# Performance work log

Measured on AMD Instinct MI355X. Metric: run time of the kernel, lower is better.

Reference implementation:

```python
import jax, jax.numpy as jnp
import numpy as np

B, S, H = 1, 2048, 2048
NH, NKV, HD = 32, 4, 128
G = NH // NKV            # query groups per kv head
EPS = 1e-6
THETA = 1000000.0


def _rmsnorm(x, w):
    # per-head RMSNorm over last (head_dim) axis
    var = jnp.mean(jnp.square(x), axis=-1, keepdims=True)
    return x * jax.lax.rsqrt(var + EPS) * w


def _rotate_half(x):
    x1, x2 = jnp.split(x, 2, axis=-1)
    return jnp.concatenate([-x2, x1], axis=-1)


def _rope(x, cos, sin):
    # x: [B,S,h,HD], cos/sin: [S,HD]
    c = cos[None, :, None, :]
    s = sin[None, :, None, :]
    return x * c + _rotate_half(x) * s


def setup_inputs() -> dict:
    key = jax.random.key(0)
    ks = jax.random.split(key, 7)
    inv_freq = 1.0 / (THETA ** (jnp.arange(0, HD, 2, dtype=jnp.float32) / HD))
    freqs = jnp.outer(jnp.arange(S, dtype=jnp.float32), inv_freq)  # [S, HD/2]
    emb = jnp.concatenate([freqs, freqs], axis=-1)                 # [S, HD]
    std = 0.02
    return {
        "hidden_states": jax.random.normal(ks[0], (B, S, H), jnp.float32),
        "wq": jax.random.normal(ks[1], (H, NH * HD), jnp.float32) * std,
        "wk": jax.random.normal(ks[2], (H, NKV * HD), jnp.float32) * std,
        "wv": jax.random.normal(ks[3], (H, NKV * HD), jnp.float32) * std,
        "wo": jax.random.normal(ks[4], (NH * HD, H), jnp.float32) * std,
        "q_norm_w": jnp.ones((HD,), jnp.float32),
        "k_norm_w": jnp.ones((HD,), jnp.float32),
        "cos": jnp.cos(emb),
        "sin": jnp.sin(emb),
    }


def reference(hidden_states, wq, wk, wv, wo, q_norm_w, k_norm_w, cos, sin):
    b, s, _ = hidden_states.shape
    q = (hidden_states @ wq).reshape(b, s, NH, HD)
    k = (hidden_states @ wk).reshape(b, s, NKV, HD)
    v = (hidden_states @ wv).reshape(b, s, NKV, HD)
    # QK per-head RMSNorm, then interleaved RoPE (rotate-half form)
    q = _rope(_rmsnorm(q, q_norm_w), cos, sin)
    k = _rope(_rmsnorm(k, k_norm_w), cos, sin)
    # GQA: group Q heads per KV head instead of materializing repeated K/V
    qg = q.reshape(b, s, NKV, G, HD)
    scaling = HD ** -0.5
    scores = jnp.einsum('bqhgd,bkhd->bhgqk', qg, k) * scaling  # [B,NKV,G,S,S]
    causal = jnp.tril(jnp.ones((s, s), bool))
    scores = jnp.where(causal, scores, jnp.finfo(scores.dtype).min)
    p = jax.nn.softmax(scores, axis=-1)
    attn = jnp.einsum('bhgqk,bkhd->bqhgd', p, v).reshape(b, s, NH * HD)
    return attn @ wo
```

## Files before the change

### kernel.cpp

```cpp
#include <hip/hip_runtime.h>
#include <hip/hip_bf16.h>
#include <stdint.h>

#define SEQ 2048
#define HDIM 128
#define NHEADS 32
#define NKVH 4

typedef unsigned short u16;
typedef __bf16 bf16_t;
typedef bf16_t bf16x8 __attribute__((ext_vector_type(8)));
typedef float floatx4 __attribute__((ext_vector_type(4)));

__device__ __forceinline__ float bf2f(u16 u) {
  union { uint32_t i; float f; } v; v.i = ((uint32_t)u) << 16; return v.f;
}
__device__ __forceinline__ u16 f2bf(float f) {
  if (__builtin_isnan(f)) return 0;
  union { float f; uint32_t i; } v; v.f = f;
  uint32_t r = v.i + 0x7fffu + ((v.i >> 16) & 1u);
  return (u16)(r >> 16);
}
__device__ __forceinline__ float loadf_any(const void* p, size_t i, int isbf) {
  return isbf ? bf2f(((const u16*)p)[i]) : ((const float*)p)[i];
}

__device__ __forceinline__ void gload_lds16(const u16* g, u16* l) {
  __builtin_amdgcn_global_load_lds((__attribute__((address_space(1))) void*)g,
                                   (__attribute__((address_space(3))) void*)l,
                                   16, 0, 0);
}

__device__ __forceinline__ floatx4 mfma16(bf16x8 a, bf16x8 b, floatx4 c) {
  return __builtin_amdgcn_mfma_f32_16x16x32_bf16(a, b, c, 0, 0, 0);
}

struct InPack { const u16* p[9]; int n[9]; };

__global__ void detect_all(InPack pk, int* __restrict__ flags) {
  const int which = blockIdx.x;
  const u16* x = pk.p[which];
  const int n = pk.n[which];
  __shared__ int s_sane, s_zeven, s_zodd;
  if (threadIdx.x == 0) { s_sane = 0; s_zeven = 0; s_zodd = 0; }
  __syncthreads();
  const int ns = n < 8192 ? n : 8192;
  int sane = 0, zeven = 0, zodd = 0;
  for (int i = threadIdx.x; i < ns; i += 256) {
    const u16 u = x[i];
    const int e = (u >> 7) & 0xff;
    if ((e >= 96 && e <= 159) || u == 0) sane++;
    if (u == 0) { if (i & 1) zodd++; else zeven++; }
  }
#pragma unroll
  for (int off = 32; off >= 1; off >>= 1) {
    sane += __shfl_xor(sane, off, 64);
    zeven += __shfl_xor(zeven, off, 64);
    zodd += __shfl_xor(zodd, off, 64);
  }
  if ((threadIdx.x & 63) == 0) {
    atomicAdd(&s_sane, sane);
    atomicAdd(&s_zeven, zeven);
    atomicAdd(&s_zodd, zodd);
  }
  __syncthreads();
  if (threadIdx.x == 0) {
    const int even = (ns + 1) / 2, odd = ns / 2;
    const bool mostly_sane = (s_sane * 10 >= ns * 9);
    const bool fp32_const_pattern = (s_zeven * 2 >= even) && (s_zodd * 10 <= odd);
    flags[which] = (mostly_sane && !fp32_const_pattern) ? 1 : 0;
    if (which == 0) flags[15] = 1;
  }
}

__global__ __launch_bounds__(256) void convert_any(
    const void* __restrict__ in, u16* __restrict__ out, int n,
    const int* __restrict__ flag) {
  const int isbf = *flag;
  const int i = blockIdx.x * 256 + threadIdx.x;
  if (i >= n) return;
  out[i] = isbf ? ((const u16*)in)[i] : f2bf(((const float*)in)[i]);
}

__global__ __launch_bounds__(256) void transpose_any(
    const void* __restrict__ in, u16* __restrict__ out, int R, int C,
    const int* __restrict__ flag) {
  __shared__ u16 tile[64][65];
  const int isbf = *flag;
  const int c0 = blockIdx.x * 64, r0 = blockIdx.y * 64;
  const int t = threadIdx.x;
#pragma unroll
  for (int i = 0; i < 16; i++) {
    const int idx = i * 256 + t;
    const int r = idx >> 6, c = idx & 63;
    tile[r][c] = (u16)(isbf ? ((const u16*)in)[(size_t)(r0 + r) * C + c0 + c]
                            : f2bf(((const float*)in)[(size_t)(r0 + r) * C + c0 + c]));
  }
  __syncthreads();
#pragma unroll
  for (int i = 0; i < 16; i++) {
    const int idx = i * 256 + t;
    const int cc = idx >> 6, rr = idx & 63;
    out[(size_t)(c0 + cc) * R + r0 + rr] = tile[rr][cc];
  }
}

__global__ __launch_bounds__(256) void gemm_bt_bf16(
    const u16* __restrict__ A, const u16* __restrict__ BT,
    void* __restrict__ C, int M, int N, int K,
    const int* __restrict__ cflag) {
  __shared__ alignas(16) u16 As[128 * 32];
  __shared__ alignas(16) u16 Bs[128 * 32];
  const int t = threadIdx.x;
  const int w = t >> 6;
  const int lane = t & 63;
  const int lhi = lane >> 4, llo = lane & 15;
  const int m0 = blockIdx.y * 128, n0 = blockIdx.x * 128;
  const int wm = (w & 1) * 64, wn = (w >> 1) * 64;

  floatx4 acc[4][4];
#pragma unroll
  for (int i = 0; i < 4; i++)
#pragma unroll
    for (int j = 0; j < 4; j++) acc[i][j] = (floatx4)(0.0f);

  for (int k0 = 0; k0 < K; k0 += 32) {
#pragma unroll
    for (int r = 0; r < 2; r++) {
      const int c = r * 256 + t;
      const int row = c >> 2, kc = c & 3;
      const int base = (r * 256 + w * 64) * 8;
      gload_lds16(A + (size_t)(m0 + row) * K + k0 + kc * 8, &As[base]);
      gload_lds16(BT + (size_t)(n0 + row) * K + k0 + kc * 8, &Bs[base]);
    }
    __syncthreads();
    bf16x8 af[4], bfr[4];
#pragma unroll
    for (int i = 0; i < 4; i++)
      af[i] = *(const bf16x8*)&As[(wm + i * 16 + llo) * 32 + lhi * 8];
#pragma unroll
    for (int j = 0; j < 4; j++)
      bfr[j] = *(const bf16x8*)&Bs[(wn + j * 16 + llo) * 32 + lhi * 8];
#pragma unroll
    for (int i = 0; i < 4; i++)
#pragma unroll
      for (int j = 0; j < 4; j++)
        acc[i][j] = mfma16(af[i], bfr[j], acc[i][j]);
    __syncthreads();
  }
  const int cbf = *cflag;
#pragma unroll
  for (int i = 0; i < 4; i++) {
    const int row0 = m0 + wm + i * 16 + lhi * 4;
#pragma unroll
    for (int j = 0; j < 4; j++) {
      const int col = n0 + wn + j * 16 + llo;
#pragma unroll
      for (int r = 0; r < 4; r++) {
        if (cbf) ((u16*)C)[(size_t)(row0 + r) * N + col] = f2bf(acc[i][j][r]);
        else ((float*)C)[(size_t)(row0 + r) * N + col] = acc[i][j][r];
      }
    }
  }
}

__global__ __launch_bounds__(128) void norm_rope_inplace(
    u16* __restrict__ QKV,
    const void* __restrict__ qw, const void* __restrict__ kw,
    const void* __restrict__ cosb, const void* __restrict__ sinb,
    const int* __restrict__ flags) {
  const int qwbf = flags[5], kwbf = flags[6], cbf = flags[7], sbf = flags[8];
  const int s = blockIdx.x, hy = blockIdx.y, d = threadIdx.x;
  const bool isQ = hy < NHEADS;
  const int col = isQ ? hy * HDIM : 4096 + (hy - NHEADS) * HDIM;
  u16* ptr = QKV + (size_t)s * 5120 + col + d;
  const float x = bf2f(*ptr);
  float v = x * x;
#pragma unroll
  for (int off = 32; off >= 1; off >>= 1) v += __shfl_xor(v, off, 64);
  __shared__ float sw[2];
  __shared__ float sh[128];
  if ((d & 63) == 0) sw[d >> 6] = v;
  __syncthreads();
  const float mean = (sw[0] + sw[1]) * (1.0f / 128.0f);
  const float rn = rsqrtf(mean + 1e-6f);
  const float wv = isQ ? loadf_any(qw, d, qwbf) : loadf_any(kw, d, kwbf);
  const float xn = x * rn * wv;
  sh[d] = xn;
  __syncthreads();
  const float other = sh[d ^ 64];
  const float cv = loadf_any(cosb, (size_t)s * HDIM + d, cbf);
  const float sv = loadf_any(sinb, (size_t)s * HDIM + d, sbf);
  const float o = xn * cv + (d < 64 ? -other : other) * sv;
  *ptr = f2bf(o);
}

__global__ __launch_bounds__(256) void v_transpose(
    const u16* __restrict__ QKV, u16* __restrict__ Vt) {
  __shared__ u16 tile[64][65];
  const int s0 = blockIdx.x * 64, d0 = blockIdx.y * 64, hk = blockIdx.z;
  const int t = threadIdx.x;
#pragma unroll
  for (int i = 0; i < 16; i++) {
    const int idx = i * 256 + t;
    const int r = idx >> 6, c = idx & 63;
    tile[r][c] = QKV[(size_t)(s0 + r) * 5120 + 4608 + hk * HDIM + d0 + c];
  }
  __syncthreads();
#pragma unroll
  for (int i = 0; i < 16; i++) {
    const int idx = i * 256 + t;
    const int dd = idx >> 6, ss = idx & 63;
    Vt[((size_t)hk * HDIM + d0 + dd) * SEQ + s0 + ss] = tile[ss][dd];
  }
}

__global__ __launch_bounds__(256) void flash_attn(
    const u16* __restrict__ QKV, const u16* __restrict__ Vt,
    u16* __restrict__ O) {
  __shared__ alignas(16) u16 Klds[64 * 128];
  __shared__ alignas(16) u16 Vlds[128 * 64];
  __shared__ alignas(16) u16 Plds[4][32 * 72];
  const int t = threadIdx.x;
  const int w = t >> 6;
  const int lane = t & 63;
  const int lhi = lane >> 4, llo = lane & 15;
  const int b = blockIdx.x;
  const int qt = (SEQ / 128 - 1) - (b >> 5);
  const int h = b & 31, hk = h >> 3;
  const int q0 = qt * 128;
  const int qw0 = q0 + w * 32;
  const float scale = 0.08838834764831845f;
  const float SMAX = 16.0f;

  bf16x8 qf[2][4];
#pragma unroll
  for (int i = 0; i < 2; i++)
#pragma unroll
    for (int c = 0; c < 4; c++)
      qf[i][c] = *(const bf16x8*)(QKV + (size_t)(qw0 + i * 16 + llo) * 5120 +
                                  h * HDIM + c * 32 + lhi * 8);

  floatx4 oacc[2][8];
  float lacc[2][4];
#pragma unroll
  for (int i = 0; i < 2; i++) {
#pragma unroll
    for (int d = 0; d < 8; d++) oacc[i][d] = (floatx4)(0.0f);
#pragma unroll
    for (int r = 0; r < 4; r++) lacc[i][r] = 0.0f;
  }

  const int ntiles = 2 * qt + 2;
  for (int tt = 0; tt < ntiles; tt++) {
    const int kv0 = tt * 64;
#pragma unroll
    for (int r = 0; r < 4; r++) {
      const int c = r * 256 + t;
      const int base = (r * 256 + w * 64) * 8;
      gload_lds16(QKV + (size_t)(kv0 + (c >> 4)) * 5120 + 4096 + hk * HDIM +
                      (((c & 15) ^ ((c >> 4) & 7)) * 8),
                  &Klds[base]);
      gload_lds16(Vt + ((size_t)hk * HDIM + (c >> 3)) * SEQ + kv0 +
                      (((c & 7) ^ ((c >> 3) & 7)) * 8),
                  &Vlds[base]);
    }
    __syncthreads();

    floatx4 sacc[2][4];
#pragma unroll
    for (int i = 0; i < 2; i++)
#pragma unroll
      for (int j = 0; j < 4; j++) sacc[i][j] = (floatx4)(0.0f);
#pragma unroll
    for (int j = 0; j < 4; j++) {
#pragma unroll
      for (int c = 0; c < 4; c++) {
        bf16x8 kf = *(const bf16x8*)&Klds[(j * 16 + llo) * 128 +
                                          (((c * 4 + lhi) ^ (llo & 7)) * 8)];
        sacc[0][j] = mfma16(qf[0][c], kf, sacc[0][j]);
        sacc[1][j] = mfma16(qf[1][c], kf, sacc[1][j]);
      }
    }
    if (kv0 + 64 > q0) {
#pragma unroll
      for (int i = 0; i < 2; i++)
#pragma unroll
        for (int j = 0; j < 4; j++) {
          const int n = kv0 + j * 16 + llo;
#pragma unroll
          for (int r = 0; r < 4; r++) {
            const int mm = qw0 + i * 16 + lhi * 4 + r;
            if (n > mm) sacc[i][j][r] = -30000.0f;
          }
        }
    }
#pragma unroll
    for (int i = 0; i < 2; i++)
#pragma unroll
      for (int j = 0; j < 4; j++)
#pragma unroll
        for (int r = 0; r < 4; r++) {
          const float p = __expf(fmaf(sacc[i][j][r], scale, -SMAX));
          lacc[i][r] += p;
          Plds[w][(i * 16 + lhi * 4 + r) * 72 + j * 16 + llo] = f2bf(p);
        }
    asm volatile("" ::: "memory");
    __builtin_amdgcn_s_waitcnt(0);
    asm volatile("" ::: "memory");
#pragma unroll
    for (int c = 0; c < 2; c++) {
      bf16x8 pf0 = *(const bf16x8*)&Plds[w][llo * 72 + c * 32 + lhi * 8];
      bf16x8 pf1 = *(const bf16x8*)&Plds[w][(16 + llo) * 72 + c * 32 + lhi * 8];
#pragma unroll
      for (int d = 0; d < 8; d++) {
        bf16x8 vf = *(const bf16x8*)&Vlds[(d * 16 + llo) * 64 +
                                          (((c * 4 + lhi) ^ (llo & 7)) * 8)];
        oacc[0][d] = mfma16(pf0, vf, oacc[0][d]);
        oacc[1][d] = mfma16(pf1, vf, oacc[1][d]);
      }
    }
    __syncthreads();
  }
#pragma unroll
  for (int i = 0; i < 2; i++)
#pragma unroll
    for (int r = 0; r < 4; r++) {
#pragma unroll
      for (int off = 1; off < 16; off <<= 1)
        lacc[i][r] += __shfl_xor(lacc[i][r], off, 64);
      const float linv = 1.0f / lacc[i][r];
      const int row = qw0 + i * 16 + lhi * 4 + r;
#pragma unroll
      for (int d = 0; d < 8; d++)
        O[(size_t)row * 4096 + h * HDIM + d * 16 + llo] =
            f2bf(oacc[i][d][r] * linv);
    }
}

extern "C" void kernel_launch(void* const* d_in, const int* in_sizes, int n_in,
                              void* d_out, int out_size, void* d_ws, size_t ws_size,
                              hipStream_t stream) {
  char* ws = (char*)d_ws;
  u16* wqkvT  = (u16*)(ws);
  u16* QKVp   = (u16*)(ws + (20ull << 20));
  u16* Vt     = (u16*)(ws + (40ull << 20));
  int* flags  = (int*)(ws + (42ull << 20));
  u16* attnO  = wqkvT;
  u16* woT    = QKVp;
  u16* Hb     = (u16*)d_out;

  InPack pk;
  for (int i = 0; i < 9; i++) { pk.p[i] = (const u16*)d_in[i]; pk.n[i] = in_sizes[i]; }
  detect_all<<<9, 256, 0, stream>>>(pk, flags);

  convert_any<<<(2048 * 2048) / 256, 256, 0, stream>>>(d_in[0], Hb, 2048 * 2048, flags + 0);
  transpose_any<<<dim3(64, 32), 256, 0, stream>>>(d_in[1], wqkvT, 2048, 4096, flags + 1);
  transpose_any<<<dim3(8, 32), 256, 0, stream>>>(d_in[2], wqkvT + 4096ull * 2048, 2048, 512, flags + 2);
  transpose_any<<<dim3(8, 32), 256, 0, stream>>>(d_in[3], wqkvT + 4608ull * 2048, 2048, 512, flags + 3);

  gemm_bt_bf16<<<dim3(40, 16), 256, 0, stream>>>(
      Hb, wqkvT, QKVp, 2048, 5120, 2048, flags + 15);

  norm_rope_inplace<<<dim3(2048, NHEADS + NKVH), 128, 0, stream>>>(
      QKVp, d_in[5], d_in[6], d_in[7], d_in[8], flags);
  v_transpose<<<dim3(32, 2, 4), 256, 0, stream>>>(QKVp, Vt);

  flash_attn<<<512, 256, 0, stream>>>(QKVp, Vt, attnO);

  transpose_any<<<dim3(32, 64), 256, 0, stream>>>(d_in[4], woT, 4096, 2048, flags + 4);
  gemm_bt_bf16<<<dim3(16, 16), 256, 0, stream>>>(
      attnO, woT, d_out, 2048, 2048, 4096, flags + 0);
}
```

Measured before the change: 455.0 us.

## Fuse input prep kernels and use intra-block split-K for output projection

Merges the hidden-state conversion and the three weight transposes into a single prep_all launch, cutting launch overhead and tail effects. The output projection GEMM now runs as 1024-thread blocks, where four 256-thread groups each handle a quarter of K and reduce through shared memory. This raises the number of waves per tile for the 256-tile grid, at the cost of a serialized LDS reduction and 64KB of shared memory per block. The P-tile store in flash attention also switches to a native bf16 conversion.

Result: faster. 399.6 us (-12.2%).

```diff
diff --git a/kernel.cpp b/kernel.cpp
--- a/kernel.cpp
+++ b/kernel.cpp
@@ -73,21 +73,10 @@
   }
 }
 
-__global__ __launch_bounds__(256) void convert_any(
-    const void* __restrict__ in, u16* __restrict__ out, int n,
-    const int* __restrict__ flag) {
-  const int isbf = *flag;
-  const int i = blockIdx.x * 256 + threadIdx.x;
-  if (i >= n) return;
-  out[i] = isbf ? ((const u16*)in)[i] : f2bf(((const float*)in)[i]);
-}
-
-__global__ __launch_bounds__(256) void transpose_any(
-    const void* __restrict__ in, u16* __restrict__ out, int R, int C,
-    const int* __restrict__ flag) {
-  __shared__ u16 tile[64][65];
-  const int isbf = *flag;
-  const int c0 = blockIdx.x * 64, r0 = blockIdx.y * 64;
+__device__ __forceinline__ void transpose_tile(
+    u16 (&tile)[64][65], const void* __restrict__ in, u16* __restrict__ out,
+    int R, int C, int isbf, int bx, int by) {
+  const int c0 = bx * 64, r0 = by * 64;
   const int t = threadIdx.x;
 #pragma unroll
   for (int i = 0; i < 16; i++) {
@@ -103,6 +92,41 @@
     const int cc = idx >> 6, rr = idx & 63;
     out[(size_t)(c0 + cc) * R + r0 + rr] = tile[rr][cc];
   }
+}
+
+__global__ __launch_bounds__(256) void prep_all(
+    const void* __restrict__ hs, const void* __restrict__ wq,
+    const void* __restrict__ wk, const void* __restrict__ wv,
+    u16* __restrict__ Hb, u16* __restrict__ wqkvT,
+    const int* __restrict__ flags) {
+  __shared__ u16 tile[64][65];
+  const int b = blockIdx.x;
+  if (b < 2048) {
+    transpose_tile(tile, wq, wqkvT, 2048, 4096, flags[1], b & 63, b >> 6);
+  } else if (b < 2304) {
+    const int r = b - 2048;
+    transpose_tile(tile, wk, wqkvT + 4096ull * 2048, 2048, 512, flags[2],
+                   r & 7, r >> 3);
+  } else if (b < 2560) {
+    const int r = b - 2304;
+    transpose_tile(tile, wv, wqkvT + 4608ull * 2048, 2048, 512, flags[3],
+                   r & 7, r >> 3);
+  } else {
+    const int r = b - 2560;
+    const int isbf = flags[0];
+#pragma unroll
+    for (int i = 0; i < 4; i++) {
+      const int idx = (r * 4 + i) * 256 + threadIdx.x;
+      Hb[idx] = isbf ? ((const u16*)hs)[idx] : f2bf(((const float*)hs)[idx]);
+    }
+  }
+}
+
+__global__ __launch_bounds__(256) void transpose_any(
+    const void* __restrict__ in, u16* __restrict__ out, int R, int C,
+    const int* __restrict__ flag) {
+  __shared__ u16 tile[64][65];
+  transpose_tile(tile, in, out, R, C, *flag, blockIdx.x, blockIdx.y);
 }
 
 __global__ __launch_bounds__(256) void gemm_bt_bf16(
@@ -161,6 +185,84 @@
         else ((float*)C)[(size_t)(row0 + r) * N + col] = acc[i][j][r];
       }
     }
+  }
+}
+
+__global__ __launch_bounds__(1024) void gemm_bt_splitk(
+    const u16* __restrict__ A, const u16* __restrict__ BT,
+    void* __restrict__ C, int M, int N, int K,
+    const int* __restrict__ cflag) {
+  __shared__ alignas(16) u16 smem[4][2][128 * 32];
+  const int t = threadIdx.x;
+  const int g = t >> 8;
+  const int tg = t & 255;
+  const int w = tg >> 6;
+  const int lane = t & 63;
+  const int lhi = lane >> 4, llo = lane & 15;
+  const int m0 = blockIdx.y * 128, n0 = blockIdx.x * 128;
+  const int wm = (w & 1) * 64, wn = (w >> 1) * 64;
+  const int kq = K >> 2;
+  const int kbeg = g * kq;
+  u16* As = smem[g][0];
+  u16* Bs = smem[g][1];
+
+  floatx4 acc[4][4];
+#pragma unroll
+  for (int i = 0; i < 4; i++)
+#pragma unroll
+    for (int j = 0; j < 4; j++) acc[i][j] = (floatx4)(0.0f);
+
+  for (int k0 = 0; k0 < kq; k0 += 32) {
+#pragma unroll
+    for (int r = 0; r < 2; r++) {
+      const int c = r * 256 + tg;
+      const int row = c >> 2, kc = c & 3;
+      const int base = (r * 256 + w * 64) * 8;
+      gload_lds16(A + (size_t)(m0 + row) * K + kbeg + k0 + kc * 8, &As[base]);
+      gload_lds16(BT + (size_t)(n0 + row) * K + kbeg + k0 + kc * 8, &Bs[base]);
+    }
+    __syncthreads();
+    bf16x8 af[4], bfr[4];
+#pragma unroll
+    for (int i = 0; i < 4; i++)
+      af[i] = *(const bf16x8*)&As[(wm + i * 16 + llo) * 32 + lhi * 8];
+#pragma unroll
+    for (int j = 0; j < 4; j++)
+      bfr[j] = *(const bf16x8*)&Bs[(wn + j * 16 + llo) * 32 + lhi * 8];
+#pragma unroll
+    for (int i = 0; i < 4; i++)
+#pragma unroll
+      for (int j = 0; j < 4; j++)
+        acc[i][j] = mfma16(af[i], bfr[j], acc[i][j]);
+    __syncthreads();
+  }
+
+  float* red = (float*)&smem[0][0][0];
+  for (int gg = 0; gg < 4; gg++) {
+    if (g == gg) {
+#pragma unroll
+      for (int i = 0; i < 4; i++)
+#pragma unroll
+        for (int j = 0; j < 4; j++) {
+          const int col = wn + j * 16 + llo;
+#pragma unroll
+          for (int r = 0; r < 4; r++) {
+            const int row = wm + i * 16 + lhi * 4 + r;
+            if (gg == 0) red[row * 128 + col] = acc[i][j][r];
+            else red[row * 128 + col] += acc[i][j][r];
+          }
+        }
+    }
+    __syncthreads();
+  }
+  const int cbf = *cflag;
+#pragma unroll
+  for (int i = 0; i < 16; i++) {
+    const int idx = i * 1024 + t;
+    const int rr = idx >> 7, cc = idx & 127;
+    const float v = red[rr * 128 + cc];
+    if (cbf) ((u16*)C)[(size_t)(m0 + rr) * N + n0 + cc] = f2bf(v);
+    else ((float*)C)[(size_t)(m0 + rr) * N + n0 + cc] = v;
   }
 }
 
@@ -303,7 +405,8 @@
         for (int r = 0; r < 4; r++) {
           const float p = __expf(fmaf(sacc[i][j][r], scale, -SMAX));
           lacc[i][r] += p;
-          Plds[w][(i * 16 + lhi * 4 + r) * 72 + j * 16 + llo] = f2bf(p);
+          *(bf16_t*)&Plds[w][(i * 16 + lhi * 4 + r) * 72 + j * 16 + llo] =
+              (bf16_t)p;
         }
     asm volatile("" ::: "memory");
     __builtin_amdgcn_s_waitcnt(0);
@@ -354,10 +457,8 @@
   for (int i = 0; i < 9; i++) { pk.p[i] = (const u16*)d_in[i]; pk.n[i] = in_sizes[i]; }
   detect_all<<<9, 256, 0, stream>>>(pk, flags);
 
-  convert_any<<<(2048 * 2048) / 256, 256, 0, stream>>>(d_in[0], Hb, 2048 * 2048, flags + 0);
-  transpose_any<<<dim3(64, 32), 256, 0, stream>>>(d_in[1], wqkvT, 2048, 4096, flags + 1);
-  transpose_any<<<dim3(8, 32), 256, 0, stream>>>(d_in[2], wqkvT + 4096ull * 2048, 2048, 512, flags + 2);
-  transpose_any<<<dim3(8, 32), 256, 0, stream>>>(d_in[3], wqkvT + 4608ull * 2048, 2048, 512, flags + 3);
+  prep_all<<<6656, 256, 0, stream>>>(
+      d_in[0], d_in[1], d_in[2], d_in[3], Hb, wqkvT, flags);
 
   gemm_bt_bf16<<<dim3(40, 16), 256, 0, stream>>>(
       Hb, wqkvT, QKVp, 2048, 5120, 2048, flags + 15);
@@ -369,6 +470,6 @@
   flash_attn<<<512, 256, 0, stream>>>(QKVp, Vt, attnO);
 
   transpose_any<<<dim3(32, 64), 256, 0, stream>>>(d_in[4], woT, 4096, 2048, flags + 4);
-  gemm_bt_bf16<<<dim3(16, 16), 256, 0, stream>>>(
+  gemm_bt_splitk<<<dim3(16, 16), 1024, 0, stream>>>(
       attnO, woT, d_out, 2048, 2048, 4096, flags + 0);
 }
```
